# Performance work log

Measured on AMD Instinct MI355X. Metric: run time of the kernel, lower is better.

## Reference

```python
import jax, jax.numpy as jnp
import numpy as np
import math

B, T = 64, 2000
RNN_DIM, EMB_DIM, ATT_DIM = 1024, 512, 128
STATIC_CH, STATIC_K = 8, 21
DYN_CH, DYN_K = 8, 21
PRIOR_LEN, ALPHA, BETA = 11, 0.1, 0.9


def _betabinom_pmf(k, n, a, b):
    lg = math.lgamma
    return math.exp(lg(n + 1) - lg(k + 1) - lg(n - k + 1)
                    + lg(k + a) + lg(n - k + b) - lg(n + a + b)
                    - (lg(a) + lg(b) - lg(a + b)))


def setup_inputs() -> dict:
    key = jax.random.key(0)
    ks = jax.random.split(key, 12)
    query = jax.random.normal(ks[0], (B, RNN_DIM), jnp.float32)
    memory = jax.random.normal(ks[1], (B, T, EMB_DIM), jnp.float32)
    a = jax.random.uniform(ks[2], (B, T), jnp.float32)
    alignment_pre = a / jnp.sum(a, axis=1, keepdims=True)  # valid attention distribution
    mask = jnp.zeros((B, T), dtype=bool)
    s = 1.0 / math.sqrt(RNN_DIM)
    W_w = jax.random.uniform(ks[3], (ATT_DIM, RNN_DIM), jnp.float32, -s, s)
    W_b = jax.random.uniform(ks[4], (ATT_DIM,), jnp.float32, -s, s)
    V_w = jax.random.normal(ks[5], (DYN_CH * DYN_K, ATT_DIM), jnp.float32) * 0.05
    F_w = jax.random.normal(ks[6], (STATIC_CH, 1, STATIC_K), jnp.float32) * 0.1
    U_w = jax.random.normal(ks[7], (ATT_DIM, STATIC_CH), jnp.float32) * 0.1
    T_w = jax.random.normal(ks[8], (ATT_DIM, DYN_CH), jnp.float32) * 0.1
    T_b = jax.random.normal(ks[9], (ATT_DIM,), jnp.float32) * 0.05
    v_w = jax.random.normal(ks[10], (1, ATT_DIM), jnp.float32) * 0.1
    P_np = np.array([_betabinom_pmf(k, PRIOR_LEN - 1, ALPHA, BETA) for k in range(PRIOR_LEN)], np.float32)
    P = jnp.asarray(P_np[::-1].copy())  # buffer: flipped beta-binomial prior
    return {"attention_hidden_state": query, "memory": memory, "alignment_pre": alignment_pre,
            "mask": mask, "W_w": W_w, "W_b": W_b, "V_w": V_w, "F_w": F_w,
            "U_w": U_w, "T_w": T_w, "T_b": T_b, "v_w": v_w, "P": P}


def _conv1d(lhs, rhs, pad, groups=1):
    # lhs [N,C,T], rhs [O,C//groups,K]; cross-correlation, matching torch conv1d
    return jax.lax.conv_general_dilated(lhs, rhs, (1,), [pad],
                                        dimension_numbers=("NCH", "OIH", "NCH"),
                                        feature_group_count=groups)


def reference(attention_hidden_state, memory, alignment_pre, mask,
              W_w, W_b, V_w, F_w, U_w, T_w, T_b, v_w, P):
    b, t = alignment_pre.shape
    # log of causal beta-binomial prior: left-pad by prior_length-1, valid conv
    p = _conv1d(alignment_pre[:, None, :], P.reshape(1, 1, -1), (PRIOR_LEN - 1, 0))[:, 0, :]
    p = jnp.log(jnp.clip(p, 1e-6))
    # per-sample dynamic kernels: [B, dyn_ch*K]
    G = jnp.tanh(attention_hidden_state @ W_w.T + W_b) @ V_w.T
    g = _conv1d(alignment_pre[None, :, :], G.reshape(b * DYN_CH, 1, DYN_K),
                ((DYN_K - 1) // 2, (DYN_K - 1) // 2), groups=b)  # [1, B*dyn_ch, T]
    g = g.reshape(b, DYN_CH, t).transpose(0, 2, 1)  # [B, T, dyn_ch]
    # static conv features
    f = _conv1d(alignment_pre[:, None, :], F_w,
                ((STATIC_K - 1) // 2, (STATIC_K - 1) // 2)).transpose(0, 2, 1)  # [B, T, static_ch]
    e = (jnp.tanh(f @ U_w.T + g @ T_w.T + T_b) @ v_w.T)[..., 0] + p  # [B, T]
    e = jnp.where(mask, -jnp.inf, e)
    attention_weights = jax.nn.softmax(e, axis=1)
    attention_context = jnp.einsum("bt,bte->be", attention_weights, memory)
    return attention_context, attention_weights
```

## Files before the change

kernel.cpp:

```cpp
#include <hip/hip_runtime.h>

#define B_    64
#define T_    2000
#define RNN_  1024
#define EMB_  512
#define ATT_  128
#define CH_   8
#define K_    21
#define PL_   11
#define GSZ   168
#define NCH   16
#define CROWS 125
#define MAGIC 0x13371337u

typedef float vf4 __attribute__((ext_vector_type(4)));

__device__ __forceinline__ float fast_tanh(float x) {
    float ax = fabsf(x);
    float e  = __expf(2.0f * ax);
    float t  = 1.0f - 2.0f / (e + 1.0f);
    return copysignf(t, x);
}

__global__ __launch_bounds__(256) void k_gen_dyn(
    const float* __restrict__ q, const float* __restrict__ Ww,
    const float* __restrict__ Wb, const float* __restrict__ Vw,
    float* __restrict__ G, float* __restrict__ out_ctx)
{
    __shared__ float sq[RNN_];
    __shared__ float part[256];
    __shared__ float sh[ATT_];
    const int b = blockIdx.x, tid = threadIdx.x;
    for (int i = tid; i < EMB_; i += 256) out_ctx[b * EMB_ + i] = 0.f;
    for (int i = tid; i < RNN_; i += 256) sq[i] = q[b * RNN_ + i];
    __syncthreads();
    {
        const int row = tid & 127, half = tid >> 7;
        const float4* wr = reinterpret_cast<const float4*>(Ww + row * RNN_ + half * (RNN_ / 2));
        const float4* qr = reinterpret_cast<const float4*>(sq + half * (RNN_ / 2));
        float acc = 0.f;
        #pragma unroll 8
        for (int i = 0; i < RNN_ / 8; ++i) {
            float4 w4 = wr[i], q4 = qr[i];
            acc += w4.x * q4.x + w4.y * q4.y + w4.z * q4.z + w4.w * q4.w;
        }
        part[tid] = acc;
    }
    __syncthreads();
    if (tid < ATT_) sh[tid] = fast_tanh(part[tid] + part[tid + 128] + Wb[tid]);
    __syncthreads();
    for (int o = tid; o < GSZ; o += 256) {
        const float4* vr = reinterpret_cast<const float4*>(Vw + o * ATT_);
        const float4* hr = reinterpret_cast<const float4*>(sh);
        float acc = 0.f;
        #pragma unroll 8
        for (int i = 0; i < ATT_ / 4; ++i) {
            float4 v4 = vr[i], h4 = hr[i];
            acc += v4.x * h4.x + v4.y * h4.y + v4.z * h4.z + v4.w * h4.w;
        }
        G[b * GSZ + o] = acc;
    }
}

__global__ __launch_bounds__(256, 4) void k_eng_ctx(
    const float* __restrict__ a,  const float* __restrict__ G,
    const float* __restrict__ Fw, const float* __restrict__ Uw,
    const float* __restrict__ Tw, const float* __restrict__ Tb,
    const float* __restrict__ vw, const float* __restrict__ P,
    const unsigned char* __restrict__ mask, const float* __restrict__ mem,
    unsigned* __restrict__ sflag, float* __restrict__ sred,
    float* __restrict__ wout, float* __restrict__ out_ctx)
{
    __shared__ union {
        struct {
            float win[148];
            float FG[K_ * 16];
            float UT[ATT_ * 16];
            float Tb[ATT_]; float V[ATT_]; float Pr[PL_];
            float Q[256]; float red[4];
        } E;
        struct { vf4 part[2][128]; } C;
    } sm;
    __shared__ float sp[128];
    __shared__ float sS;

    const int c = blockIdx.x, b = blockIdx.y, tid = threadIdx.x;
    const int t0 = c * CROWS;
    const int tloc = tid & 127, half = tid >> 7;

    for (int j = tid; j < 148; j += 256) {
        int idx = t0 - 10 + j;
        sm.E.win[j] = (idx >= 0 && idx < T_) ? a[b * T_ + idx] : 0.f;
    }
    for (int j = tid; j < 2 * GSZ; j += 256) {
        if (j < GSZ) sm.E.FG[(j % K_) * 16 + (j / K_)] = Fw[j];
        else { int jj = j - GSZ; sm.E.FG[(jj % K_) * 16 + 8 + (jj / K_)] = G[b * GSZ + jj]; }
    }
    for (int j = tid; j < ATT_ * CH_; j += 256) {
        int d = j >> 3, ch = j & 7;
        sm.E.UT[d * 16 + ch]     = Uw[j];
        sm.E.UT[d * 16 + 8 + ch] = Tw[j];
    }
    if (tid < ATT_) { sm.E.Tb[tid] = Tb[tid]; sm.E.V[tid] = vw[tid]; }
    if (tid < PL_)  sm.E.Pr[tid] = P[tid];
    __syncthreads();

    {
        float fg[16];
        #pragma unroll
        for (int i = 0; i < 16; ++i) fg[i] = 0.f;
        #pragma unroll
        for (int k = 0; k < K_; ++k) {
            float av = sm.E.win[tloc + k];
            const vf4* fp = reinterpret_cast<const vf4*>(&sm.E.FG[k * 16]);
            vf4 x0 = fp[0], x1 = fp[1], x2 = fp[2], x3 = fp[3];
            fg[0]  += x0.x * av; fg[1]  += x0.y * av; fg[2]  += x0.z * av; fg[3]  += x0.w * av;
            fg[4]  += x1.x * av; fg[5]  += x1.y * av; fg[6]  += x1.z * av; fg[7]  += x1.w * av;
            fg[8]  += x2.x * av; fg[9]  += x2.y * av; fg[10] += x2.z * av; fg[11] += x2.w * av;
            fg[12] += x3.x * av; fg[13] += x3.y * av; fg[14] += x3.z * av; fg[15] += x3.w * av;
        }
        float accQ = 0.f;
        const int d0 = half * 64;
        #pragma unroll 4
        for (int dd = 0; dd < 64; ++dd) {
            const int d = d0 + dd;
            const vf4* up = reinterpret_cast<const vf4*>(&sm.E.UT[d * 16]);
            vf4 u0 = up[0], u1 = up[1], u2 = up[2], u3 = up[3];
            float s0 = u0.x * fg[0]  + u0.y * fg[1]  + u0.z * fg[2]  + u0.w * fg[3];
            float s1 = u1.x * fg[4]  + u1.y * fg[5]  + u1.z * fg[6]  + u1.w * fg[7];
            float s2 = u2.x * fg[8]  + u2.y * fg[9]  + u2.z * fg[10] + u2.w * fg[11];
            float s3 = u3.x * fg[12] + u3.y * fg[13] + u3.z * fg[14] + u3.w * fg[15];
            float s = (sm.E.Tb[d] + s0) + (s1 + s2) + s3;
            accQ += sm.E.V[d] * fast_tanh(s);
        }
        sm.E.Q[half * 128 + tloc] = accQ;
    }
    __syncthreads();

    float pv = 0.f;
    if (tid < CROWS) {
        const int t = t0 + tid;
        if (!mask[b * T_ + t]) {
            float pp = 0.f;
            #pragma unroll
            for (int k = 0; k < PL_; ++k) pp += sm.E.Pr[k] * sm.E.win[tid + k];
            float e = sm.E.Q[tid] + sm.E.Q[128 + tid] + __logf(fmaxf(pp, 1e-6f));
            pv = __expf(e);
        }
    }
    if (tid < 128) sp[tid] = pv;
    float ssum = pv;
    #pragma unroll
    for (int off = 32; off > 0; off >>= 1) ssum += __shfl_xor(ssum, off);
    if ((tid & 63) == 0) sm.E.red[tid >> 6] = ssum;
    __syncthreads();
    if (tid == 0) {
        float cs = sm.E.red[0] + sm.E.red[1] + sm.E.red[2] + sm.E.red[3];
        atomicExch(&sred[b * NCH + c], cs);
        __threadfence();
        atomicExch(&sflag[b * NCH + c], MAGIC);
        long long tries = 0;
        bool ok = true;
        for (int i = 0; i < NCH && ok; ++i) {
            while (atomicAdd(&sflag[b * NCH + i], 0u) != MAGIC) {
                __builtin_amdgcn_s_sleep(8);
                if (++tries > 400000ll) { ok = false; break; }
            }
        }
        float S = 0.f;
        for (int i = 0; i < NCH; ++i) S += atomicAdd(&sred[b * NCH + i], 0.f);
        sS = S;
    }
    __syncthreads();

    const float inv = 1.0f / sS;
    if (tid < CROWS) {
        float wv = sp[tid] * inv;
        sp[tid] = wv;
        wout[b * T_ + t0 + tid] = wv;
    }
    __syncthreads();

    {
        const int col = tid & 127, rp = tid >> 7;
        const float* basep = mem + ((size_t)(b * T_ + t0)) * EMB_ + col * 4;
        vf4 acc0 = {0.f, 0.f, 0.f, 0.f}, acc1 = {0.f, 0.f, 0.f, 0.f};
        #pragma unroll 8
        for (int i = 0; i < 31; ++i) {
            const int r0 = rp + 4 * i, r1 = rp + 4 * i + 2;
            vf4 m0 = *reinterpret_cast<const vf4*>(basep + (size_t)r0 * EMB_);
            vf4 m1 = *reinterpret_cast<const vf4*>(basep + (size_t)r1 * EMB_);
            acc0 += sp[r0] * m0;
            acc1 += sp[r1] * m1;
        }
        if (rp == 0) {
            vf4 m0 = *reinterpret_cast<const vf4*>(basep + (size_t)124 * EMB_);
            acc0 += sp[124] * m0;
        }
        sm.C.part[rp][col] = acc0 + acc1;
    }
    __syncthreads();
    if (tid < 128) {
        vf4 r = sm.C.part[0][tid];
        r += sm.C.part[1][tid];
        float* op = out_ctx + b * EMB_ + tid * 4;
        atomicAdd(op + 0, r.x); atomicAdd(op + 1, r.y);
        atomicAdd(op + 2, r.z); atomicAdd(op + 3, r.w);
    }
}

extern "C" void kernel_launch(void* const* d_in, const int* in_sizes, int n_in,
                              void* d_out, int out_size, void* d_ws, size_t ws_size,
                              hipStream_t stream)
{
    const float* q    = (const float*)d_in[0];
    const float* mem  = (const float*)d_in[1];
    const float* a    = (const float*)d_in[2];
    const unsigned char* mask = (const unsigned char*)d_in[3];
    const float* Ww = (const float*)d_in[4];
    const float* Wb = (const float*)d_in[5];
    const float* Vw = (const float*)d_in[6];
    const float* Fw = (const float*)d_in[7];
    const float* Uw = (const float*)d_in[8];
    const float* Tw = (const float*)d_in[9];
    const float* Tb = (const float*)d_in[10];
    const float* vw = (const float*)d_in[11];
    const float* P  = (const float*)d_in[12];

    float* out_ctx = (float*)d_out;
    float* out_w   = out_ctx + B_ * EMB_;

    float* G       = (float*)d_ws;
    float* sred    = G + B_ * GSZ;
    unsigned* sflag = (unsigned*)(sred + B_ * NCH);

    k_gen_dyn<<<B_, 256, 0, stream>>>(q, Ww, Wb, Vw, G, out_ctx);
    k_eng_ctx<<<dim3(NCH, B_), 256, 0, stream>>>(a, G, Fw, Uw, Tw, Tb, vw, P,
                                                 mask, mem, sflag, sred,
                                                 out_w, out_ctx);
}
```

Before: 101.1 us.

## Replace inter-block spin barrier with deferred softmax normalization in a final kernel

Removes the cross-block flag spin-wait used to gather softmax denominators. Each block now accumulates unnormalized exp-weighted context and partial sums, and a small final kernel scales the context and attention weights by the inverse total. Chunks shrink from 125 to 64 rows, so the grid grows to 32x64 blocks with 4-way splitting of the attention dimension. This trades a grid-wide stall for an extra launch and an extra pass over the weight buffer, and it skips max-subtraction, so exp overflow is possible if scores get large.

```diff
diff --git a/kernel.cpp b/kernel.cpp
--- a/kernel.cpp
+++ b/kernel.cpp
@@ -1,17 +1,16 @@
 #include <hip/hip_runtime.h>
 
-#define B_    64
-#define T_    2000
-#define RNN_  1024
-#define EMB_  512
-#define ATT_  128
-#define CH_   8
-#define K_    21
-#define PL_   11
-#define GSZ   168
-#define NCH   16
-#define CROWS 125
-#define MAGIC 0x13371337u
+#define B_   64
+#define T_   2000
+#define RNN_ 1024
+#define EMB_ 512
+#define ATT_ 128
+#define CH_  8
+#define K_   21
+#define PL_  11
+#define GSZ  168
+#define CCHK 64
+#define NCC  32
 
 typedef float vf4 __attribute__((ext_vector_type(4)));
 
@@ -62,35 +61,36 @@
     }
 }
 
-__global__ __launch_bounds__(256, 4) void k_eng_ctx(
+__global__ __launch_bounds__(256, 4) void k_eng_stream(
     const float* __restrict__ a,  const float* __restrict__ G,
     const float* __restrict__ Fw, const float* __restrict__ Uw,
     const float* __restrict__ Tw, const float* __restrict__ Tb,
     const float* __restrict__ vw, const float* __restrict__ P,
     const unsigned char* __restrict__ mask, const float* __restrict__ mem,
-    unsigned* __restrict__ sflag, float* __restrict__ sred,
-    float* __restrict__ wout, float* __restrict__ out_ctx)
+    float* __restrict__ pws, float* __restrict__ sred,
+    float* __restrict__ out_ctx)
 {
     __shared__ union {
         struct {
-            float win[148];
             float FG[K_ * 16];
             float UT[ATT_ * 16];
             float Tb[ATT_]; float V[ATT_]; float Pr[PL_];
-            float Q[256]; float red[4];
+            float Q[4 * CCHK]; float red[4];
         } E;
-        struct { vf4 part[2][128]; } C;
+        struct { vf4 part[2][EMB_ / 4]; } C;
     } sm;
-    __shared__ float sp[128];
-    __shared__ float sS;
-
-    const int c = blockIdx.x, b = blockIdx.y, tid = threadIdx.x;
-    const int t0 = c * CROWS;
-    const int tloc = tid & 127, half = tid >> 7;
-
-    for (int j = tid; j < 148; j += 256) {
+    __shared__ float sA[CCHK + K_ - 1];
+    __shared__ float sp[CCHK];
+
+    const int b = blockIdx.x, c = blockIdx.y, tid = threadIdx.x;
+    const int t0 = c * CCHK;
+    const int nvalid = min(CCHK, T_ - t0);
+    const int tloc = tid & (CCHK - 1);
+    const int qq = tid >> 6;
+
+    for (int j = tid; j < CCHK + K_ - 1; j += 256) {
         int idx = t0 - 10 + j;
-        sm.E.win[j] = (idx >= 0 && idx < T_) ? a[b * T_ + idx] : 0.f;
+        sA[j] = (idx >= 0 && idx < T_) ? a[b * T_ + idx] : 0.f;
     }
     for (int j = tid; j < 2 * GSZ; j += 256) {
         if (j < GSZ) sm.E.FG[(j % K_) * 16 + (j / K_)] = Fw[j];
@@ -111,7 +111,7 @@
         for (int i = 0; i < 16; ++i) fg[i] = 0.f;
         #pragma unroll
         for (int k = 0; k < K_; ++k) {
-            float av = sm.E.win[tloc + k];
+            float av = sA[tloc + k];
             const vf4* fp = reinterpret_cast<const vf4*>(&sm.E.FG[k * 16]);
             vf4 x0 = fp[0], x1 = fp[1], x2 = fp[2], x3 = fp[3];
             fg[0]  += x0.x * av; fg[1]  += x0.y * av; fg[2]  += x0.z * av; fg[3]  += x0.w * av;
@@ -120,9 +120,9 @@
             fg[12] += x3.x * av; fg[13] += x3.y * av; fg[14] += x3.z * av; fg[15] += x3.w * av;
         }
         float accQ = 0.f;
-        const int d0 = half * 64;
+        const int d0 = qq * 32;
         #pragma unroll 4
-        for (int dd = 0; dd < 64; ++dd) {
+        for (int dd = 0; dd < 32; ++dd) {
             const int d = d0 + dd;
             const vf4* up = reinterpret_cast<const vf4*>(&sm.E.UT[d * 16]);
             vf4 u0 = up[0], u1 = up[1], u2 = up[2], u3 = up[3];
@@ -133,69 +133,52 @@
             float s = (sm.E.Tb[d] + s0) + (s1 + s2) + s3;
             accQ += sm.E.V[d] * fast_tanh(s);
         }
-        sm.E.Q[half * 128 + tloc] = accQ;
+        sm.E.Q[qq * CCHK + tloc] = accQ;
     }
     __syncthreads();
 
     float pv = 0.f;
-    if (tid < CROWS) {
+    if (tid < CCHK) {
         const int t = t0 + tid;
-        if (!mask[b * T_ + t]) {
+        if (t < T_ && !mask[b * T_ + min(t, T_ - 1)]) {
             float pp = 0.f;
             #pragma unroll
-            for (int k = 0; k < PL_; ++k) pp += sm.E.Pr[k] * sm.E.win[tid + k];
-            float e = sm.E.Q[tid] + sm.E.Q[128 + tid] + __logf(fmaxf(pp, 1e-6f));
+            for (int k = 0; k < PL_; ++k) pp += sm.E.Pr[k] * sA[tid + k];
+            float e = (sm.E.Q[tid] + sm.E.Q[CCHK + tid])
+                    + (sm.E.Q[2 * CCHK + tid] + sm.E.Q[3 * CCHK + tid])
+                    + __logf(fmaxf(pp, 1e-6f));
             pv = __expf(e);
         }
-    }
-    if (tid < 128) sp[tid] = pv;
+        sp[tid] = pv;
+        if (t0 + tid < T_) pws[b * T_ + t0 + tid] = pv;
+    }
     float ssum = pv;
     #pragma unroll
     for (int off = 32; off > 0; off >>= 1) ssum += __shfl_xor(ssum, off);
     if ((tid & 63) == 0) sm.E.red[tid >> 6] = ssum;
     __syncthreads();
-    if (tid == 0) {
-        float cs = sm.E.red[0] + sm.E.red[1] + sm.E.red[2] + sm.E.red[3];
-        atomicExch(&sred[b * NCH + c], cs);
-        __threadfence();
-        atomicExch(&sflag[b * NCH + c], MAGIC);
-        long long tries = 0;
-        bool ok = true;
-        for (int i = 0; i < NCH && ok; ++i) {
-            while (atomicAdd(&sflag[b * NCH + i], 0u) != MAGIC) {
-                __builtin_amdgcn_s_sleep(8);
-                if (++tries > 400000ll) { ok = false; break; }
-            }
-        }
-        float S = 0.f;
-        for (int i = 0; i < NCH; ++i) S += atomicAdd(&sred[b * NCH + i], 0.f);
-        sS = S;
-    }
-    __syncthreads();
-
-    const float inv = 1.0f / sS;
-    if (tid < CROWS) {
-        float wv = sp[tid] * inv;
-        sp[tid] = wv;
-        wout[b * T_ + t0 + tid] = wv;
-    }
+    if (tid == 0)
+        sred[b * NCC + c] = sm.E.red[0] + sm.E.red[1] + sm.E.red[2] + sm.E.red[3];
     __syncthreads();
 
     {
         const int col = tid & 127, rp = tid >> 7;
         const float* basep = mem + ((size_t)(b * T_ + t0)) * EMB_ + col * 4;
         vf4 acc0 = {0.f, 0.f, 0.f, 0.f}, acc1 = {0.f, 0.f, 0.f, 0.f};
-        #pragma unroll 8
-        for (int i = 0; i < 31; ++i) {
-            const int r0 = rp + 4 * i, r1 = rp + 4 * i + 2;
-            vf4 m0 = *reinterpret_cast<const vf4*>(basep + (size_t)r0 * EMB_);
-            vf4 m1 = *reinterpret_cast<const vf4*>(basep + (size_t)r1 * EMB_);
-            acc0 += sp[r0] * m0;
-            acc1 += sp[r1] * m1;
-        }
-        if (rp == 0) {
-            vf4 m0 = *reinterpret_cast<const vf4*>(basep + (size_t)124 * EMB_);
-            acc0 += sp[124] * m0;
+        if (nvalid == CCHK) {
+            #pragma unroll
+            for (int i = 0; i < CCHK / 4; ++i) {
+                const int r0 = rp + 4 * i, r1 = rp + 4 * i + 2;
+                vf4 m0 = *reinterpret_cast<const vf4*>(basep + (size_t)r0 * EMB_);
+                vf4 m1 = *reinterpret_cast<const vf4*>(basep + (size_t)r1 * EMB_);
+                acc0 += sp[r0] * m0;
+                acc1 += sp[r1] * m1;
+            }
+        } else {
+            for (int tt = rp; tt < nvalid; tt += 2) {
+                vf4 mv = *reinterpret_cast<const vf4*>(basep + (size_t)tt * EMB_);
+                acc0 += sp[tt] * mv;
+            }
         }
         sm.C.part[rp][col] = acc0 + acc1;
     }
@@ -207,6 +190,22 @@
         atomicAdd(op + 0, r.x); atomicAdd(op + 1, r.y);
         atomicAdd(op + 2, r.z); atomicAdd(op + 3, r.w);
     }
+}
+
+__global__ __launch_bounds__(256) void k_final(
+    const float* __restrict__ sred, const float* __restrict__ pws,
+    float* __restrict__ out_ctx, float* __restrict__ out_w)
+{
+    __shared__ float sS;
+    const int b = blockIdx.x, tid = threadIdx.x;
+    float v = (tid < NCC) ? sred[b * NCC + tid] : 0.f;
+    #pragma unroll
+    for (int off = 16; off > 0; off >>= 1) v += __shfl_xor(v, off);
+    if (tid == 0) sS = v;
+    __syncthreads();
+    const float inv = 1.0f / sS;
+    for (int i = tid; i < EMB_; i += 256) out_ctx[b * EMB_ + i] *= inv;
+    for (int j = tid; j < T_; j += 256) out_w[b * T_ + j] = pws[b * T_ + j] * inv;
 }
 
 extern "C" void kernel_launch(void* const* d_in, const int* in_sizes, int n_in,
@@ -230,12 +229,12 @@
     float* out_ctx = (float*)d_out;
     float* out_w   = out_ctx + B_ * EMB_;
 
-    float* G       = (float*)d_ws;
-    float* sred    = G + B_ * GSZ;
-    unsigned* sflag = (unsigned*)(sred + B_ * NCH);
+    float* G    = (float*)d_ws;
+    float* sred = G + B_ * GSZ;
+    float* pws  = sred + B_ * NCC;
 
     k_gen_dyn<<<B_, 256, 0, stream>>>(q, Ww, Wb, Vw, G, out_ctx);
-    k_eng_ctx<<<dim3(NCH, B_), 256, 0, stream>>>(a, G, Fw, Uw, Tw, Tb, vw, P,
-                                                 mask, mem, sflag, sred,
-                                                 out_w, out_ctx);
-}
+    k_eng_stream<<<dim3(B_, NCC), 256, 0, stream>>>(a, G, Fw, Uw, Tw, Tb, vw, P,
+                                                    mask, mem, pws, sred, out_ctx);
+    k_final<<<B_, 256, 0, stream>>>(sred, pws, out_ctx, out_w);
+}
```

After: 85.12 us. -15.8%, faster.
